# Kernel tuning notes

Hardware: AMD Instinct MI355X
Metric: run time of the kernel (lower is better)

The kernel has to match this reference:

```python
import jax, jax.numpy as jnp
import numpy as np

B, N_O, N_Q = 2, 512, 512
POS_DIM, LATENT, HEADS, HEAD_DIM, OUT_DIM = 3, 256, 8, 32, 128
HD = HEADS * HEAD_DIM  # == LATENT here


def _lin(key, fan_in, fan_out):
    return jax.random.normal(key, (fan_in, fan_out), jnp.float32) / np.sqrt(fan_in)


def setup_inputs() -> dict:
    key = jax.random.key(0)
    ks = jax.random.split(key, 12)
    return {
        'h_obs': jax.random.normal(ks[0], (B, N_O, LATENT), jnp.float32),
        'pos_obs': jax.random.uniform(ks[1], (B, N_O, POS_DIM), jnp.float32),
        'pos_query': jax.random.uniform(ks[2], (B, N_Q, POS_DIM), jnp.float32),
        'fw1': _lin(ks[3], LATENT, LATENT), 'fb1': jnp.zeros((LATENT,), jnp.float32),
        'fw2': _lin(ks[4], LATENT, HD), 'fb2': jnp.zeros((HD,), jnp.float32),
        'log_sigma': jnp.zeros((HEADS,), jnp.float32),
        'kw1': _lin(ks[5], POS_DIM * 3, LATENT), 'kb1': jnp.zeros((LATENT,), jnp.float32),
        'kw2': _lin(ks[6], LATENT, HEADS), 'kb2': jnp.zeros((HEADS,), jnp.float32),
        'ow': _lin(ks[7], HD, OUT_DIM), 'ob': jnp.zeros((OUT_DIM,), jnp.float32),
        'vw': _lin(ks[8], HD, OUT_DIM), 'vb': jnp.zeros((OUT_DIM,), jnp.float32),
    }


def reference(h_obs, pos_obs, pos_query, fw1, fb1, fw2, fb2, log_sigma,
              kw1, kb1, kw2, kb2, ow, ob, vw, vb):
    Bv, No, _ = h_obs.shape
    Nq = pos_query.shape[1]
    # feature net -> values [B, H, N_o, D]
    v = jax.nn.relu(h_obs @ fw1 + fb1) @ fw2 + fb2
    v = v.reshape(Bv, No, HEADS, HEAD_DIM).transpose(0, 2, 1, 3)
    # pairwise relative positions [B, Nq, No, P]
    pos_q = pos_query[:, :, None, :]
    pos_o = pos_obs[:, None, :, :]
    rel = pos_q - pos_o
    dist2 = jnp.sum(rel ** 2, axis=-1)  # [B, Nq, No]
    sigma = jnp.exp(log_sigma)[None, :, None, None]
    rbf = jnp.exp(-dist2[:, None] / (sigma ** 2 + 1e-6))  # [B, H, Nq, No]
    # kernel MLP on concatenated pairwise positions [B, Nq, No, 3P] -> [B, H, Nq, No]
    ki = jnp.concatenate([
        jnp.broadcast_to(pos_q, (Bv, Nq, No, POS_DIM)),
        jnp.broadcast_to(pos_o, (Bv, Nq, No, POS_DIM)),
        rel], axis=-1)
    delta = (jax.nn.relu(ki @ kw1 + kb1) @ kw2 + kb2).transpose(0, 3, 1, 2)
    logits = jnp.log(rbf + 1e-8) + delta
    weights = jax.nn.softmax(logits, axis=-1)  # [B, H, Nq, No]
    # weighted mean over observations
    v_mean = jnp.einsum('bhqo,bhod->bhqd', weights, v)  # [B, H, Nq, D]
    h_query = v_mean.transpose(0, 2, 1, 3).reshape(Bv, Nq, HD)
    # weighted variance: sum_o w * (v_o - v_mean)^2
    residual = v[:, :, None, :, :] - v_mean[:, :, :, None, :]  # [B, H, Nq, No, D]
    var = jnp.sum(weights[..., None] * residual ** 2, axis=3)  # [B, H, Nq, D]
    var = var.transpose(0, 2, 1, 3).reshape(Bv, Nq, HD)
    mean = h_query @ ow + ob
    var_out = jax.nn.softplus(var @ vw + vb)
    return (mean, var_out)
```

## Files before the change

### kernel.cpp

```cpp
#include <hip/hip_runtime.h>
#include <math.h>

#define NB 2
#define NO 512
#define NQ 512
#define OUT_DIM 128
#define LPAD 516

typedef __attribute__((ext_vector_type(8))) _Float16 half8;
typedef __attribute__((ext_vector_type(4))) _Float16 half4;
typedef __attribute__((ext_vector_type(4))) float f32x4;

__device__ __forceinline__ float softplus_f(float x) {
  return x > 0.0f ? x + log1pf(expf(-x)) : log1pf(expf(x));
}
__device__ __forceinline__ half8 splat8(_Float16 v) {
  return (half8){v, v, v, v, v, v, v, v};
}
__device__ __forceinline__ half8 fma8(half8 a, half8 b, half8 c) {
  return __builtin_elementwise_fma(a, b, c);
}
__device__ __forceinline__ half8 max8(half8 a, half8 b) {
  return __builtin_elementwise_max(a, b);
}
__device__ __forceinline__ void gll16(const void* g, void* l) {
  __builtin_amdgcn_global_load_lds(
      (const __attribute__((address_space(1))) unsigned int*)g,
      (__attribute__((address_space(3))) unsigned int*)l, 16, 0, 0);
}

__global__ __launch_bounds__(1024) void prep_kernel(
    const float* __restrict__ h_obs, const float* __restrict__ fw1,
    const float* __restrict__ fb1, const float* __restrict__ fw2,
    const float* __restrict__ fb2, _Float16* __restrict__ VT)
{
  __shared__ float s_red[4][4][256];
  __shared__ float s_hid[4][256];
  const int n  = threadIdx.x & 255;
  const int ks = threadIdx.x >> 8;
  const int r0 = blockIdx.x * 4;
  const int k0 = ks * 64;
  float a0 = 0.f, a1 = 0.f, a2 = 0.f, a3 = 0.f;
  #pragma unroll 8
  for (int kk = 0; kk < 64; ++kk) {
    int k = k0 + kk;
    float w = fw1[k * 256 + n];
    a0 = fmaf(h_obs[(r0 + 0) * 256 + k], w, a0);
    a1 = fmaf(h_obs[(r0 + 1) * 256 + k], w, a1);
    a2 = fmaf(h_obs[(r0 + 2) * 256 + k], w, a2);
    a3 = fmaf(h_obs[(r0 + 3) * 256 + k], w, a3);
  }
  s_red[ks][0][n] = a0; s_red[ks][1][n] = a1;
  s_red[ks][2][n] = a2; s_red[ks][3][n] = a3;
  __syncthreads();
  if (ks == 0) {
    float bb = fb1[n];
    #pragma unroll
    for (int r = 0; r < 4; ++r) {
      float v = s_red[0][r][n] + s_red[1][r][n] + s_red[2][r][n] + s_red[3][r][n] + bb;
      s_hid[r][n] = fmaxf(v, 0.f);
    }
  }
  __syncthreads();
  float c0 = 0.f, c1 = 0.f, c2 = 0.f, c3 = 0.f;
  #pragma unroll 8
  for (int kk = 0; kk < 64; ++kk) {
    int k = k0 + kk;
    float w = fw2[k * 256 + n];
    c0 = fmaf(s_hid[0][k], w, c0);
    c1 = fmaf(s_hid[1][k], w, c1);
    c2 = fmaf(s_hid[2][k], w, c2);
    c3 = fmaf(s_hid[3][k], w, c3);
  }
  __syncthreads();
  s_red[ks][0][n] = c0; s_red[ks][1][n] = c1;
  s_red[ks][2][n] = c2; s_red[ks][3][n] = c3;
  __syncthreads();
  if (ks == 0) {
    float bb = fb2[n];
    float vr[4];
    #pragma unroll
    for (int r = 0; r < 4; ++r)
      vr[r] = s_red[0][r][n] + s_red[1][r][n] + s_red[2][r][n] + s_red[3][r][n] + bb;
    const int h  = n >> 5, d = n & 31;
    const int bb_ = r0 >> 9, o0 = r0 & 511;
    half4 pv;
    #pragma unroll
    for (int r = 0; r < 4; ++r) pv[r] = (_Float16)vr[r];
    *(half4*)(VT + ((size_t)((bb_ * 8 + h) * 32 + d)) * 512 + o0) = pv;
  }
}

__global__ __launch_bounds__(512, 4) void attn_fused(
    const _Float16* __restrict__ VT,
    const float* __restrict__ kw1,
    const float* __restrict__ kb1,
    const float* __restrict__ kw2,
    const float* __restrict__ kb2,
    const float* __restrict__ log_sigma,
    const float* __restrict__ pos_obs,
    const float* __restrict__ pos_query,
    const float* __restrict__ ow, const float* __restrict__ obias,
    const float* __restrict__ vw, const float* __restrict__ vbias,
    float* __restrict__ out)
{
  __shared__ __align__(16) float s_logits[2][8 * LPAD];
  __shared__ __align__(16) _Float16 s_P16[2][8][520];
  __shared__ half8 s_Bh[512];
  __shared__ __align__(16) float s_pool[2048];
  __shared__ __align__(16) float s_po[3][516];
  __shared__ __align__(16) _Float16 s_co[3][264];

  _Float16* s_aq2 = (_Float16*)s_pool;
  float*    s_hv   = s_pool;
  float*    s_pred = s_pool + 1024;

  const int t   = threadIdx.x;
  const int bq0 = blockIdx.x * 2;
  const int b   = bq0 >> 9;

  float pqx[2], pqy[2], pqz[2];
  #pragma unroll
  for (int q = 0; q < 2; ++q) {
    pqx[q] = pos_query[(bq0 + q) * 3 + 0];
    pqy[q] = pos_query[(bq0 + q) * 3 + 1];
    pqz[q] = pos_query[(bq0 + q) * 3 + 2];
  }
  {
    const int q = t >> 8, j = t & 255;
    float c0 = kw1[0 * 256 + j] + kw1[6 * 256 + j];
    float c1 = kw1[1 * 256 + j] + kw1[7 * 256 + j];
    float c2 = kw1[2 * 256 + j] + kw1[8 * 256 + j];
    s_aq2[q * 256 + j] = (_Float16)
        fmaf(pqx[q], c0, fmaf(pqy[q], c1, fmaf(pqz[q], c2, kb1[j])));
  }
  if (t < 256) {
    const int j = t;
    s_co[0][j] = (_Float16)(kw1[3 * 256 + j] - kw1[6 * 256 + j]);
    s_co[1][j] = (_Float16)(kw1[4 * 256 + j] - kw1[7 * 256 + j]);
    s_co[2][j] = (_Float16)(kw1[5 * 256 + j] - kw1[8 * 256 + j]);
  }
  {
    const int o = t;
    const float* p = pos_obs + (size_t)(b * NO + o) * 3;
    float px = p[0], py = p[1], pz = p[2];
    s_po[0][o] = px; s_po[1][o] = py; s_po[2][o] = pz;
    float d2q[2];
    #pragma unroll
    for (int q = 0; q < 2; ++q) {
      float r0 = pqx[q] - px, r1 = pqy[q] - py, r2 = pqz[q] - pz;
      d2q[q] = r0 * r0 + r1 * r1 + r2 * r2;
    }
    #pragma unroll
    for (int h = 0; h < 8; ++h) {
      float sg  = __expf(log_sigma[h]);
      float inv = 1.0f / (sg * sg + 1e-6f);
      float kbv = kb2[h];
      s_logits[0][h * LPAD + o] = fmaxf(-d2q[0] * inv, -18.420681f) + kbv;
      s_logits[1][h * LPAD + o] = fmaxf(-d2q[1] * inv, -18.420681f) + kbv;
    }
  }
  {
    const int kstep = t >> 6, lane = t & 63;
    const int nh = lane & 15;
    const int kb_ = kstep * 32 + ((lane >> 4) & 3) * 8;
    half8 b8;
    #pragma unroll
    for (int i = 0; i < 8; ++i) {
      float v = (nh < 8) ? kw2[(kb_ + i) * 8 + nh] : 0.f;
      b8[i] = (_Float16)v;
    }
    s_Bh[kstep * 64 + lane] = b8;
  }
  __syncthreads();

  {
    const int wave = t >> 6, lane = t & 63;
    const int quad = lane >> 4, mrow = lane & 15;
    const int tb   = wave * 4;
    _Float16 pxh[4], pyh[4], pzh[4];
    #pragma unroll
    for (int jt = 0; jt < 4; ++jt) {
      const int o = (tb + jt) * 16 + mrow;
      pxh[jt] = (_Float16)s_po[0][o];
      pyh[jt] = (_Float16)s_po[1][o];
      pzh[jt] = (_Float16)s_po[2][o];
    }
    f32x4 C[2][4];
    #pragma unroll
    for (int q = 0; q < 2; ++q)
      #pragma unroll
      for (int jt = 0; jt < 4; ++jt) C[q][jt] = (f32x4){0.f, 0.f, 0.f, 0.f};

    const half8 z8 = {0, 0, 0, 0, 0, 0, 0, 0};
    #pragma unroll
    for (int kstep = 0; kstep < 8; ++kstep) {
      const int koff = kstep * 32 + quad * 8;
      half8 c0 = *(const half8*)&s_co[0][koff];
      half8 c1 = *(const half8*)&s_co[1][koff];
      half8 c2 = *(const half8*)&s_co[2][koff];
      half8 aq0 = *(const half8*)(s_aq2 + koff);
      half8 aq1 = *(const half8*)(s_aq2 + 256 + koff);
      half8 bh  = s_Bh[kstep * 64 + lane];
      #pragma unroll
      for (int jt = 0; jt < 4; ++jt) {
        half8 ao = fma8(splat8(pxh[jt]), c0,
                   fma8(splat8(pyh[jt]), c1, splat8(pzh[jt]) * c2));
        half8 a0 = max8(aq0 + ao, z8);
        half8 a1 = max8(aq1 + ao, z8);
        C[0][jt] = __builtin_amdgcn_mfma_f32_16x16x32_f16(a0, bh, C[0][jt], 0, 0, 0);
        C[1][jt] = __builtin_amdgcn_mfma_f32_16x16x32_f16(a1, bh, C[1][jt], 0, 0, 0);
      }
    }
    const int hh = lane & 15;
    if (hh < 8) {
      #pragma unroll
      for (int q = 0; q < 2; ++q)
        #pragma unroll
        for (int jt = 0; jt < 4; ++jt) {
          const int ob2 = (tb + jt) * 16 + quad * 4;
          #pragma unroll
          for (int r = 0; r < 4; ++r)
            s_logits[q][hh * LPAD + ob2 + r] += C[q][jt][r];
        }
    }
  }
  __syncthreads();

  {
    const int h = t >> 6, lane = t & 63;
    const int kg = lane >> 4, dl = lane & 15;
    char* stg0 = (char*)s_Bh + h * 1024;
    char* b1   = (char*)&s_logits[0][h * LPAD];
    char* b3   = b1 + 1024;
    char* b2   = (char*)&s_logits[1][h * LPAD];
    const _Float16* vsrc = VT + ((size_t)(b * 8 + h) << 14)
                         + (lane >> 1) * 512 + (lane & 1) * 8;
    gll16(vsrc, stg0);

    float invq0, invq1;
    {
      const float* pl0 = &s_logits[0][h * LPAD];
      const float* pl1 = &s_logits[1][h * LPAD];
      float l0[8], l1[8];
      float m0 = -1e30f, m1 = -1e30f;
      #pragma unroll
      for (int k = 0; k < 8; ++k) {
        l0[k] = pl0[k * 64 + lane];
        l1[k] = pl1[k * 64 + lane];
        m0 = fmaxf(m0, l0[k]);
        m1 = fmaxf(m1, l1[k]);
      }
      #pragma unroll
      for (int off = 32; off >= 1; off >>= 1) {
        m0 = fmaxf(m0, __shfl_xor(m0, off, 64));
        m1 = fmaxf(m1, __shfl_xor(m1, off, 64));
      }
      float s0 = 0.f, s1 = 0.f;
      _Float16* pp0 = &s_P16[0][h][0];
      _Float16* pp1 = &s_P16[1][h][0];
      #pragma unroll
      for (int k = 0; k < 8; ++k) {
        float p0 = __expf(l0[k] - m0);
        float p1 = __expf(l1[k] - m1);
        s0 += p0; s1 += p1;
        pp0[k * 64 + lane] = (_Float16)p0;
        pp1[k * 64 + lane] = (_Float16)p1;
      }
      #pragma unroll
      for (int off = 32; off >= 1; off >>= 1) {
        s0 += __shfl_xor(s0, off, 64);
        s1 += __shfl_xor(s1, off, 64);
      }
      invq0 = 1.0f / s0; invq1 = 1.0f / s1;
    }
    gll16(vsrc + 16, b1);
    gll16(vsrc + 32, b2);
    gll16(vsrc + 48, b3);

    const char* pE = ((kg & 2) ? b1 : stg0) + dl * 32 + (kg & 1) * 16;
    const char* pO = ((kg & 2) ? b3 : b2)   + dl * 32 + (kg & 1) * 16;
    const _Float16* pB = &s_P16[lane & 1][h][0];
    f32x4 Cm0 = {0.f, 0.f, 0.f, 0.f}, Cm1 = Cm0, Cv0 = Cm0, Cv1 = Cm0;
    #pragma unroll
    for (int kp = 0; kp < 8; ++kp) {
      asm volatile("s_waitcnt vmcnt(2)" ::: "memory");
      {
        half8 am0 = *(const half8*)(pE);
        half8 am1 = *(const half8*)(pE + 512);
        half8 pb  = *(const half8*)(pB + (2 * kp) * 32 + kg * 8);
        half8 av0 = am0 * am0;
        half8 av1 = am1 * am1;
        __builtin_amdgcn_s_setprio(1);
        Cm0 = __builtin_amdgcn_mfma_f32_16x16x32_f16(am0, pb, Cm0, 0, 0, 0);
        Cm1 = __builtin_amdgcn_mfma_f32_16x16x32_f16(am1, pb, Cm1, 0, 0, 0);
        Cv0 = __builtin_amdgcn_mfma_f32_16x16x32_f16(av0, pb, Cv0, 0, 0, 0);
        Cv1 = __builtin_amdgcn_mfma_f32_16x16x32_f16(av1, pb, Cv1, 0, 0, 0);
        __builtin_amdgcn_s_setprio(0);
      }
      if (kp < 7) {
        asm volatile("s_waitcnt lgkmcnt(0)" ::: "memory");
        gll16(vsrc + (4 * kp + 4) * 16, stg0);
        gll16(vsrc + (4 * kp + 5) * 16, b1);
      }
      if (kp < 7) asm volatile("s_waitcnt vmcnt(2)" ::: "memory");
      else        asm volatile("s_waitcnt vmcnt(0)" ::: "memory");
      {
        half8 am0 = *(const half8*)(pO);
        half8 am1 = *(const half8*)(pO + 512);
        half8 pb  = *(const half8*)(pB + (2 * kp + 1) * 32 + kg * 8);
        half8 av0 = am0 * am0;
        half8 av1 = am1 * am1;
        __builtin_amdgcn_s_setprio(1);
        Cm0 = __builtin_amdgcn_mfma_f32_16x16x32_f16(am0, pb, Cm0, 0, 0, 0);
        Cm1 = __builtin_amdgcn_mfma_f32_16x16x32_f16(am1, pb, Cm1, 0, 0, 0);
        Cv0 = __builtin_amdgcn_mfma_f32_16x16x32_f16(av0, pb, Cv0, 0, 0, 0);
        Cv1 = __builtin_amdgcn_mfma_f32_16x16x32_f16(av1, pb, Cv1, 0, 0, 0);
        __builtin_amdgcn_s_setprio(0);
      }
      if (kp < 7) {
        asm volatile("s_waitcnt lgkmcnt(0)" ::: "memory");
        gll16(vsrc + (4 * kp + 6) * 16, b2);
        gll16(vsrc + (4 * kp + 7) * 16, b3);
      }
    }
    const int nq = lane & 15;
    if (nq < 2) {
      const float iv = nq ? invq1 : invq0;
      const int dbase = h * 32 + kg * 4;
      f32x4 m0, v0, m1, v1;
      #pragma unroll
      for (int r = 0; r < 4; ++r) {
        float a = Cm0[r] * iv;
        m0[r] = a; v0[r] = fmaxf(Cv0[r] * iv - a * a, 0.f);
        float c = Cm1[r] * iv;
        m1[r] = c; v1[r] = fmaxf(Cv1[r] * iv - c * c, 0.f);
      }
      *(f32x4*)(s_hv + (nq * 2 + 0) * 256 + dbase)      = m0;
      *(f32x4*)(s_hv + (nq * 2 + 1) * 256 + dbase)      = v0;
      *(f32x4*)(s_hv + (nq * 2 + 0) * 256 + dbase + 16) = m1;
      *(f32x4*)(s_hv + (nq * 2 + 1) * 256 + dbase + 16) = v1;
    }
  }
  __syncthreads();

  {
    const int ks = t >> 8, mode = (t >> 7) & 1, n = t & 127;
    const float* W  = mode ? vw : ow;
    const float* X0 = s_hv + mode * 256;
    const float* X1 = s_hv + (2 + mode) * 256;
    float a0 = 0.f, a1 = 0.f;
    const int k0 = ks * 128;
    #pragma unroll 4
    for (int k = k0; k < k0 + 128; k += 4) {
      float4 x0 = *(const float4*)&X0[k];
      float4 x1 = *(const float4*)&X1[k];
      float w0 = W[(k + 0) * 128 + n];
      float w1 = W[(k + 1) * 128 + n];
      float w2 = W[(k + 2) * 128 + n];
      float w3 = W[(k + 3) * 128 + n];
      a0 = fmaf(x0.x, w0, a0); a1 = fmaf(x1.x, w0, a1);
      a0 = fmaf(x0.y, w1, a0); a1 = fmaf(x1.y, w1, a1);
      a0 = fmaf(x0.z, w2, a0); a1 = fmaf(x1.z, w2, a1);
      a0 = fmaf(x0.w, w3, a0); a1 = fmaf(x1.w, w3, a1);
    }
    s_pred[((ks * 2 + mode) * 2 + 0) * 128 + n] = a0;
    s_pred[((ks * 2 + mode) * 2 + 1) * 128 + n] = a1;
  }
  __syncthreads();
  {
    const int q = t >> 8, mode = (t >> 7) & 1, n = t & 127;
    float v = s_pred[((0 * 2 + mode) * 2 + q) * 128 + n]
            + s_pred[((1 * 2 + mode) * 2 + q) * 128 + n]
            + (mode ? vbias[n] : obias[n]);
    if (mode) v = softplus_f(v);
    out[(size_t)mode * (NB * NQ * OUT_DIM) + (size_t)(bq0 + q) * OUT_DIM + n] = v;
  }
}

extern "C" void kernel_launch(void* const* d_in, const int* in_sizes, int n_in,
                              void* d_out, int out_size, void* d_ws, size_t ws_size,
                              hipStream_t stream)
{
  const float* h_obs     = (const float*)d_in[0];
  const float* pos_obs   = (const float*)d_in[1];
  const float* pos_query = (const float*)d_in[2];
  const float* fw1       = (const float*)d_in[3];
  const float* fb1       = (const float*)d_in[4];
  const float* fw2       = (const float*)d_in[5];
  const float* fb2       = (const float*)d_in[6];
  const float* log_sigma = (const float*)d_in[7];
  const float* kw1       = (const float*)d_in[8];
  const float* kb1       = (const float*)d_in[9];
  const float* kw2       = (const float*)d_in[10];
  const float* kb2       = (const float*)d_in[11];
  const float* ow        = (const float*)d_in[12];
  const float* ob        = (const float*)d_in[13];
  const float* vw        = (const float*)d_in[14];
  const float* vb        = (const float*)d_in[15];

  float* out = (float*)d_out;
  _Float16* VT = (_Float16*)d_ws;

  prep_kernel<<<256, 1024, 0, stream>>>(h_obs, fw1, fb1, fw2, fb2, VT);
  attn_fused<<<NB * NQ / 2, 512, 0, stream>>>(VT, kw1, kb1, kw2, kb2,
                                              log_sigma, pos_obs, pos_query,
                                              ow, ob, vw, vb, out);
}
```

Measured before the change: 125.3 us.

## Split output projection out of attention kernel into separate proj kernel

Moves the final mean/variance projections (ow, vw) and softplus out of the fused attention kernel. The attention kernel now writes its per-query mean and variance vectors to a global workspace, and a new kernel projects 8 queries per block. This cuts shared memory in the attention kernel (s_pool shrinks from 2048 to 256 floats), which may allow more resident blocks, and lets each weight load be reused across more queries. In exchange it adds a kernel launch and a round trip through global memory for the intermediate vectors.

```diff
diff --git a/kernel.cpp b/kernel.cpp
--- a/kernel.cpp
+++ b/kernel.cpp
@@ -100,20 +100,16 @@
     const float* __restrict__ log_sigma,
     const float* __restrict__ pos_obs,
     const float* __restrict__ pos_query,
-    const float* __restrict__ ow, const float* __restrict__ obias,
-    const float* __restrict__ vw, const float* __restrict__ vbias,
-    float* __restrict__ out)
+    float* __restrict__ HVg)
 {
   __shared__ __align__(16) float s_logits[2][8 * LPAD];
   __shared__ __align__(16) _Float16 s_P16[2][8][520];
   __shared__ half8 s_Bh[512];
-  __shared__ __align__(16) float s_pool[2048];
+  __shared__ __align__(16) float s_pool[256];
   __shared__ __align__(16) float s_po[3][516];
   __shared__ __align__(16) _Float16 s_co[3][264];
 
   _Float16* s_aq2 = (_Float16*)s_pool;
-  float*    s_hv   = s_pool;
-  float*    s_pred = s_pool + 1024;
 
   const int t   = threadIdx.x;
   const int bq0 = blockIdx.x * 2;
@@ -336,45 +332,43 @@
         float c = Cm1[r] * iv;
         m1[r] = c; v1[r] = fmaxf(Cv1[r] * iv - c * c, 0.f);
       }
-      *(f32x4*)(s_hv + (nq * 2 + 0) * 256 + dbase)      = m0;
-      *(f32x4*)(s_hv + (nq * 2 + 1) * 256 + dbase)      = v0;
-      *(f32x4*)(s_hv + (nq * 2 + 0) * 256 + dbase + 16) = m1;
-      *(f32x4*)(s_hv + (nq * 2 + 1) * 256 + dbase + 16) = v1;
-    }
-  }
-  __syncthreads();
-
-  {
-    const int ks = t >> 8, mode = (t >> 7) & 1, n = t & 127;
-    const float* W  = mode ? vw : ow;
-    const float* X0 = s_hv + mode * 256;
-    const float* X1 = s_hv + (2 + mode) * 256;
-    float a0 = 0.f, a1 = 0.f;
-    const int k0 = ks * 128;
-    #pragma unroll 4
-    for (int k = k0; k < k0 + 128; k += 4) {
-      float4 x0 = *(const float4*)&X0[k];
-      float4 x1 = *(const float4*)&X1[k];
-      float w0 = W[(k + 0) * 128 + n];
-      float w1 = W[(k + 1) * 128 + n];
-      float w2 = W[(k + 2) * 128 + n];
-      float w3 = W[(k + 3) * 128 + n];
-      a0 = fmaf(x0.x, w0, a0); a1 = fmaf(x1.x, w0, a1);
-      a0 = fmaf(x0.y, w1, a0); a1 = fmaf(x1.y, w1, a1);
-      a0 = fmaf(x0.z, w2, a0); a1 = fmaf(x1.z, w2, a1);
-      a0 = fmaf(x0.w, w3, a0); a1 = fmaf(x1.w, w3, a1);
-    }
-    s_pred[((ks * 2 + mode) * 2 + 0) * 128 + n] = a0;
-    s_pred[((ks * 2 + mode) * 2 + 1) * 128 + n] = a1;
-  }
-  __syncthreads();
-  {
-    const int q = t >> 8, mode = (t >> 7) & 1, n = t & 127;
-    float v = s_pred[((0 * 2 + mode) * 2 + q) * 128 + n]
-            + s_pred[((1 * 2 + mode) * 2 + q) * 128 + n]
-            + (mode ? vbias[n] : obias[n]);
+      float* hvq = HVg + (size_t)(bq0 + nq) * 2 * 256;
+      *(f32x4*)(hvq + 0 * 256 + dbase)      = m0;
+      *(f32x4*)(hvq + 1 * 256 + dbase)      = v0;
+      *(f32x4*)(hvq + 0 * 256 + dbase + 16) = m1;
+      *(f32x4*)(hvq + 1 * 256 + dbase + 16) = v1;
+    }
+  }
+}
+
+__global__ __launch_bounds__(256) void proj_kernel(
+    const float* __restrict__ HV,
+    const float* __restrict__ ow, const float* __restrict__ obias,
+    const float* __restrict__ vw, const float* __restrict__ vbias,
+    float* __restrict__ out)
+{
+  const int t = threadIdx.x;
+  const int mode = t >> 7, n = t & 127;
+  const int q0 = blockIdx.x * 8;
+  const float* W = mode ? vw : ow;
+  float acc[8] = {0.f, 0.f, 0.f, 0.f, 0.f, 0.f, 0.f, 0.f};
+  for (int k = 0; k < 256; k += 4) {
+    float w0 = W[(k + 0) * 128 + n];
+    float w1 = W[(k + 1) * 128 + n];
+    float w2 = W[(k + 2) * 128 + n];
+    float w3 = W[(k + 3) * 128 + n];
+    #pragma unroll
+    for (int qq = 0; qq < 8; ++qq) {
+      float4 x = *(const float4*)&HV[((size_t)(q0 + qq) * 2 + mode) * 256 + k];
+      acc[qq] = fmaf(x.w, w3, fmaf(x.z, w2, fmaf(x.y, w1, fmaf(x.x, w0, acc[qq]))));
+    }
+  }
+  const float bias = mode ? vbias[n] : obias[n];
+  #pragma unroll
+  for (int qq = 0; qq < 8; ++qq) {
+    float v = acc[qq] + bias;
     if (mode) v = softplus_f(v);
-    out[(size_t)mode * (NB * NQ * OUT_DIM) + (size_t)(bq0 + q) * OUT_DIM + n] = v;
+    out[(size_t)mode * (NB * NQ * OUT_DIM) + (size_t)(q0 + qq) * OUT_DIM + n] = v;
   }
 }
 
@@ -400,10 +394,12 @@
   const float* vb        = (const float*)d_in[15];
 
   float* out = (float*)d_out;
-  _Float16* VT = (_Float16*)d_ws;
+  _Float16* ws = (_Float16*)d_ws;
+  _Float16* VT = ws;
+  float*    HV = (float*)(ws + 262144);
 
   prep_kernel<<<256, 1024, 0, stream>>>(h_obs, fw1, fb1, fw2, fb2, VT);
   attn_fused<<<NB * NQ / 2, 512, 0, stream>>>(VT, kw1, kb1, kw2, kb2,
-                                              log_sigma, pos_obs, pos_query,
-                                              ow, ob, vw, vb, out);
-}
+                                              log_sigma, pos_obs, pos_query, HV);
+  proj_kernel<<<NB * NQ / 8, 256, 0, stream>>>(HV, ow, ob, vw, vb, out);
+}
```

After: 143.4 us. +14.4%, slower.
